# Performance work log

Hardware: AMD Instinct MI355X
Metric: run time of the kernel (lower is better)

## Reference

```python
import jax, jax.numpy as jnp
import numpy as np

N_NODES = 50000
N_EDGES = 600000
IN_DIM = 128
HID = 128


def gcn_conv(x, W, b, src, dst, num_nodes):
    """PyG-style GCNConv: add self-loops, symmetric D^-1/2 (A+I) D^-1/2 normalization."""
    xw = x @ W  # [N, H]
    loop = jnp.arange(num_nodes)
    s = jnp.concatenate([src, loop])
    d = jnp.concatenate([dst, loop])
    deg = jax.ops.segment_sum(jnp.ones_like(d, dtype=xw.dtype), d, num_segments=num_nodes)
    dinv = jax.lax.rsqrt(deg)  # deg >= 1 thanks to self-loops
    norm = dinv[s] * dinv[d]  # [E+N]
    msgs = xw[s] * norm[:, None]  # gather + scale, [E+N, H]
    out = jax.ops.segment_sum(msgs, d, num_segments=num_nodes)
    return out + b


def setup_inputs() -> dict:
    key = jax.random.key(0)
    ks = jax.random.split(key, 12)
    sc_in = 1.0 / np.sqrt(IN_DIM)
    sc_h = 1.0 / np.sqrt(HID)
    sc_2h = 1.0 / np.sqrt(2 * HID)
    return {
        "x": jax.random.normal(ks[0], (N_NODES, IN_DIM), jnp.float32),
        "hidden_state": jax.random.normal(ks[1], (N_NODES, HID), jnp.float32),
        "edge_index": jax.random.randint(ks[2], (2, N_EDGES), 0, N_NODES, dtype=jnp.int32),
        "W_in": jax.random.normal(ks[3], (IN_DIM, HID), jnp.float32) * sc_in,
        "b_in": jnp.zeros((HID,), jnp.float32),
        "W_hid": jax.random.normal(ks[4], (HID, HID), jnp.float32) * sc_h,
        "b_hid": jnp.zeros((HID,), jnp.float32),
        "W_z": jax.random.normal(ks[5], (2 * HID, HID), jnp.float32) * sc_2h,
        "b_z": jnp.zeros((HID,), jnp.float32),
        "W_r": jax.random.normal(ks[6], (2 * HID, HID), jnp.float32) * sc_2h,
        "b_r": jnp.zeros((HID,), jnp.float32),
        "W_c": jax.random.normal(ks[7], (2 * HID, HID), jnp.float32) * sc_2h,
        "b_c": jnp.zeros((HID,), jnp.float32),
    }


def reference(x, hidden_state, edge_index, W_in, b_in, W_hid, b_hid, W_z, b_z, W_r, b_r, W_c, b_c):
    src, dst = edge_index[0], edge_index[1]
    n = x.shape[0]
    # two stacked GCN layers (dropout identity in eval mode)
    h1 = jax.nn.relu(gcn_conv(x, W_in, b_in, src, dst, n))
    emb = gcn_conv(h1, W_hid, b_hid, src, dst, n)  # [N, H]
    # GRU-style gating
    combined = jnp.concatenate([emb, hidden_state], axis=1)  # [N, 2H]
    update = jax.nn.sigmoid(combined @ W_z + b_z)
    reset = jax.nn.sigmoid(combined @ W_r + b_r)
    cand_in = jnp.concatenate([emb, reset * hidden_state], axis=1)
    candidate = jnp.tanh(cand_in @ W_c + b_c)
    new_hidden = (1.0 - update) * hidden_state + update * candidate
    return new_hidden
```

## Files before the change

kernel.cpp:

```cpp
#include <hip/hip_runtime.h>
#include <cstdint>
#include <cstddef>

typedef unsigned short u16;
typedef unsigned int   u32;

typedef __bf16 bf8   __attribute__((ext_vector_type(8)));
typedef float  f32x4 __attribute__((ext_vector_type(4)));

__device__ __forceinline__ float b2f(u16 v) {
  union { u32 i; float f; } c; c.i = ((u32)v) << 16; return c.f;
}
__device__ __forceinline__ u16 f2b(float f) {
  union { u32 i; float f; } c; c.f = f;
  u32 x = c.i;
  u32 r = (x + 0x7FFFu + ((x >> 16) & 1u)) >> 16;
  return (u16)r;
}
__device__ __forceinline__ float sigf(float x) { return 1.0f / (1.0f + __expf(-x)); }
__device__ __forceinline__ float tanhfast(float x) { return 2.0f * sigf(2.0f * x) - 1.0f; }

__device__ __forceinline__ bf8 cvt8(const float* __restrict__ p) {
  f32x4 lo = *(const f32x4*)p;
  f32x4 hi = *(const f32x4*)(p + 4);
  union { u16 s[8]; bf8 v; } c;
#pragma unroll
  for (int i = 0; i < 4; ++i) { c.s[i] = f2b(lo[i]); c.s[4 + i] = f2b(hi[i]); }
  return c.v;
}
__device__ __forceinline__ bf8 asbf8(uint4 q) {
  union { uint4 q; bf8 v; } c; c.q = q; return c.v;
}

__device__ __forceinline__ void ld_lds16(const u16* g, u16* l) {
  __builtin_amdgcn_global_load_lds((const __attribute__((address_space(1))) void*)g,
                                   (__attribute__((address_space(3))) void*)l, 16, 0, 0);
}

#define CSR_STRIDE 80

__global__ __launch_bounds__(256) void k_transpose(
    const float* __restrict__ W0, const float* __restrict__ W1,
    const float* __restrict__ W2, const float* __restrict__ W3,
    const float* __restrict__ W4,
    u16* __restrict__ B0, u16* __restrict__ B1, u16* __restrict__ B2,
    u16* __restrict__ B3, u16* __restrict__ B4,
    int* __restrict__ cnt, int N) {
  if (blockIdx.x >= 64) {
    int i = (blockIdx.x - 64) * 256 + threadIdx.x;
    if (i < N) cnt[i] = 0;
    return;
  }
  int t = blockIdx.x * 256 + threadIdx.x;
  const float* in; u16* out; int f;
  if (t < 2048)       { in = W0; out = B0; f = t; }
  else if (t < 4096)  { in = W1; out = B1; f = t - 2048; }
  else if (t < 8192)  { in = W2; out = B2; f = t - 4096; }
  else if (t < 12288) { in = W3; out = B3; f = t - 8192; }
  else                { in = W4; out = B4; f = t - 12288; }
  int ln = f & 15, quad = (f >> 4) & 3, c = (f >> 6) & 7, ks = (f >> 9) & 3, hh = f >> 11;
  int n = c * 16 + ln;
  int k0 = hh * 128 + ks * 32 + quad * 8;
  union { u16 s[8]; uint4 q; } tmp;
#pragma unroll
  for (int j = 0; j < 8; ++j) tmp.s[j] = f2b(in[(size_t)(k0 + j) * 128 + n]);
  *(uint4*)(out + (size_t)f * 8) = tmp.q;
}

__global__ void k_fill(const int* __restrict__ src, const int* __restrict__ dst,
                       int* __restrict__ cnt, int* __restrict__ csr, int E) {
  int e = blockIdx.x * 256 + threadIdx.x;
  if (e < E) {
    int d = dst[e];
    int pos = atomicAdd(&cnt[d], 1);
    if (pos < CSR_STRIDE) csr[(size_t)d * CSR_STRIDE + pos] = src[e];
  }
}

__global__ __launch_bounds__(256) void k_agg(const u16* __restrict__ y,
                                             const int* __restrict__ cnt,
                                             const int* __restrict__ csr,
                                             const float* __restrict__ bias,
                                             u16* __restrict__ out, int relu, int N) {
  int wv = (blockIdx.x * 256 + threadIdx.x) >> 6;
  int lane = threadIdx.x & 63;
  if (wv >= N) return;
  int g = lane >> 4, t = lane & 15;
  const uint4* yq = (const uint4*)y;
  int deg = cnt[wv];
  int degc = (deg < 64) ? deg : 64;
  long base = (long)wv * CSR_STRIDE;
  int myidx = (lane < degc) ? csr[base + lane] : 0;

  float a[8];
#pragma unroll
  for (int j = 0; j < 8; ++j) a[j] = 0.0f;

  for (int b = 0; b < degc; b += 8) {
    int e0 = b + g, e1 = b + 4 + g;
    int s0 = __shfl(myidx, (e0 < degc) ? e0 : 0, 64);
    int s1 = __shfl(myidx, (e1 < degc) ? e1 : 0, 64);
    uint4 v0 = yq[(size_t)s0 * 16 + t];
    uint4 v1 = yq[(size_t)s1 * 16 + t];
    if (e0 < degc) {
      const u32* w = (const u32*)&v0;
#pragma unroll
      for (int i = 0; i < 4; ++i) { a[2*i] += b2f((u16)(w[i] & 0xFFFF)); a[2*i+1] += b2f((u16)(w[i] >> 16)); }
    }
    if (e1 < degc) {
      const u32* w = (const u32*)&v1;
#pragma unroll
      for (int i = 0; i < 4; ++i) { a[2*i] += b2f((u16)(w[i] & 0xFFFF)); a[2*i+1] += b2f((u16)(w[i] >> 16)); }
    }
  }
#pragma unroll
  for (int j = 0; j < 8; ++j) {
    a[j] += __shfl_xor(a[j], 16, 64);
    a[j] += __shfl_xor(a[j], 32, 64);
  }
  if (g == 0) {
    int degt = (deg < CSR_STRIDE) ? deg : CSR_STRIDE;
    for (int p = 64; p < degt; ++p) {
      int s = csr[base + p];
      uint4 v = yq[(size_t)s * 16 + t];
      const u32* w = (const u32*)&v;
#pragma unroll
      for (int i = 0; i < 4; ++i) { a[2*i] += b2f((u16)(w[i] & 0xFFFF)); a[2*i+1] += b2f((u16)(w[i] >> 16)); }
    }
    uint4 sv = yq[(size_t)wv * 16 + t];
    const u32* w = (const u32*)&sv;
#pragma unroll
    for (int i = 0; i < 4; ++i) { a[2*i] += b2f((u16)(w[i] & 0xFFFF)); a[2*i+1] += b2f((u16)(w[i] >> 16)); }
    float di = rsqrtf((float)deg + 1.0f);
    f32x4 b0 = *(const f32x4*)(bias + t * 8);
    f32x4 b1 = *(const f32x4*)(bias + t * 8 + 4);
    union { u16 s[8]; uint4 q; } o;
#pragma unroll
    for (int j = 0; j < 8; ++j) {
      float r = di * a[j] + ((j < 4) ? b0[j] : b1[j - 4]);
      if (relu) r = fmaxf(r, 0.0f);
      o.s[j] = f2b(r);
    }
    ((uint4*)out)[(size_t)wv * 16 + t] = o.q;
  }
}

template <bool AF>
__global__ __launch_bounds__(256) void k_gemm(
    const void* __restrict__ Av,
    const u16* __restrict__ Bt,
    const int* __restrict__ cnt,
    u16* __restrict__ outb, int M) {
  __shared__ __align__(16) u16 bs[16384];
  int tid = threadIdx.x;
  int lane = tid & 63, wave = tid >> 6;
  int ln = lane & 15, quad = lane >> 4;
  int rowbase = blockIdx.x * 64 + wave * 16;
  int rowA = rowbase + ln;
  long rA = (rowA < M) ? rowA : (M - 1);

  {
    const u16* g = Bt + wave * 4096 + lane * 8;
    u16* l = bs + wave * 4096;
#pragma unroll
    for (int i = 0; i < 8; ++i) ld_lds16(g + i * 512, l + i * 512);
  }

  bf8 af[4];
#pragma unroll
  for (int ks = 0; ks < 4; ++ks) {
    int kk = ks * 32 + quad * 8;
    if (AF) af[ks] = cvt8((const float*)Av + rA * 128 + kk);
    else    af[ks] = *(const bf8*)((const u16*)Av + rA * 128 + kk);
  }

  f32x4 acc[8];
#pragma unroll
  for (int c = 0; c < 8; ++c) { acc[c][0] = 0.f; acc[c][1] = 0.f; acc[c][2] = 0.f; acc[c][3] = 0.f; }

  __syncthreads();
#pragma unroll
  for (int ks = 0; ks < 4; ++ks) {
#pragma unroll
    for (int c = 0; c < 8; ++c) {
      bf8 bfr = *(const bf8*)(bs + ks * 4096 + c * 512 + lane * 8);
      acc[c] = __builtin_amdgcn_mfma_f32_16x16x32_bf16(af[ks], bfr, acc[c], 0, 0, 0);
    }
  }

  int rb = rowbase + quad * 4;
  float rs[4];
#pragma unroll
  for (int r = 0; r < 4; ++r) {
    int row = rb + r;
    rs[r] = (row < M) ? rsqrtf((float)cnt[row] + 1.0f) : 0.0f;
  }
#pragma unroll
  for (int c = 0; c < 8; ++c) {
    int col = c * 16 + ln;
#pragma unroll
    for (int r = 0; r < 4; ++r) {
      int row = rb + r;
      if (row < M) outb[(size_t)row * 128 + col] = f2b(acc[c][r] * rs[r]);
    }
  }
}

__global__ __launch_bounds__(256, 2) void k_gru(
    const u16* __restrict__ emb, const float* __restrict__ h,
    const u16* __restrict__ Btz, const u16* __restrict__ Btr, const u16* __restrict__ Btc,
    const float* __restrict__ bz, const float* __restrict__ br, const float* __restrict__ bc,
    float* __restrict__ out, int M) {
  __shared__ __align__(16) u16 at[8192];
  int tid = threadIdx.x;
  int lane = tid & 63, wave = tid >> 6;
  int ln = lane & 15, quad = lane >> 4;
  int rowbase = blockIdx.x * 64 + wave * 16;
  int rowA = rowbase + ln;
  long rA = (rowA < M) ? rowA : (M - 1);
  int rb = rowbase + quad * 4;

  const uint4* Bz = (const uint4*)Btz;
  const uint4* Br = (const uint4*)Btr;
  const uint4* Bc = (const uint4*)Btc;

  bf8 af_e[4], af_h[4];
#pragma unroll
  for (int ks = 0; ks < 4; ++ks)
    af_e[ks] = *(const bf8*)(emb + rA * 128 + ks * 32 + quad * 8);
#pragma unroll
  for (int ks = 0; ks < 4; ++ks)
    af_h[ks] = cvt8(h + rA * 128 + ks * 32 + quad * 8);

  f32x4 accz[8], accr[8];
#pragma unroll
  for (int c = 0; c < 8; ++c) {
    accz[c][0] = 0.f; accz[c][1] = 0.f; accz[c][2] = 0.f; accz[c][3] = 0.f;
    accr[c][0] = 0.f; accr[c][1] = 0.f; accr[c][2] = 0.f; accr[c][3] = 0.f;
  }

  auto loadb = [&](uint4 (&d)[8], const uint4* B, int ksg) {
#pragma unroll
    for (int c = 0; c < 8; ++c) d[c] = B[(size_t)ksg * 512 + c * 64 + lane];
  };
  auto mmzr = [&](uint4 (&cz)[8], uint4 (&cr)[8], int ksg) {
    bf8 af = (ksg < 4) ? af_e[ksg] : af_h[ksg - 4];
#pragma unroll
    for (int c = 0; c < 8; ++c) {
      accz[c] = __builtin_amdgcn_mfma_f32_16x16x32_bf16(af, asbf8(cz[c]), accz[c], 0, 0, 0);
      accr[c] = __builtin_amdgcn_mfma_f32_16x16x32_bf16(af, asbf8(cr[c]), accr[c], 0, 0, 0);
    }
  };

  uint4 z0[8], r0[8], z1[8], r1[8];
  loadb(z0, Bz, 0); loadb(r0, Br, 0);
  loadb(z1, Bz, 1); loadb(r1, Br, 1);
  mmzr(z0, r0, 0);
  loadb(z0, Bz, 2); loadb(r0, Br, 2);
  mmzr(z1, r1, 1);
  loadb(z1, Bz, 3); loadb(r1, Br, 3);
  mmzr(z0, r0, 2);
  loadb(z0, Bz, 4); loadb(r0, Br, 4);
  mmzr(z1, r1, 3);
  loadb(z1, Bz, 5); loadb(r1, Br, 5);
  mmzr(z0, r0, 4);
  loadb(z0, Bz, 6); loadb(r0, Br, 6);
  mmzr(z1, r1, 5);
  loadb(z1, Bz, 7); loadb(r1, Br, 7);
  mmzr(z0, r0, 6);
  mmzr(z1, r1, 7);

  f32x4 hc[8];
#pragma unroll
  for (int c = 0; c < 8; ++c) {
    int col = c * 16 + ln;
#pragma unroll
    for (int r = 0; r < 4; ++r) {
      int row = rb + r;
      hc[c][r] = (row < M) ? h[(size_t)row * 128 + col] : 0.0f;
    }
  }

#pragma unroll
  for (int c = 0; c < 8; ++c) {
    int col = c * 16 + ln;
    float bzc = bz[col], brc = br[col];
#pragma unroll
    for (int r = 0; r < 4; ++r) {
      float uu = sigf(accz[c][r] + bzc);
      float rr = sigf(accr[c][r] + brc);
      accz[c][r] = uu;
      int lrow = wave * 16 + quad * 4 + r;
      at[lrow * 128 + col] = f2b(rr * hc[c][r]);
      accr[c][r] = 0.0f;
    }
  }
  __syncthreads();

  bf8 af_at[4];
#pragma unroll
  for (int ks = 0; ks < 4; ++ks)
    af_at[ks] = *(const bf8*)(at + (wave * 16 + ln) * 128 + ks * 32 + quad * 8);

  auto mmc = [&](uint4 (&cc)[8], int ksg) {
    bf8 af = (ksg < 4) ? af_e[ksg] : af_at[ksg - 4];
#pragma unroll
    for (int c = 0; c < 8; ++c)
      accr[c] = __builtin_amdgcn_mfma_f32_16x16x32_bf16(af, asbf8(cc[c]), accr[c], 0, 0, 0);
  };
  uint4 c0[8], c1[8];
  loadb(c0, Bc, 0);
  loadb(c1, Bc, 1);
  mmc(c0, 0);
  loadb(c0, Bc, 2);
  mmc(c1, 1);
  loadb(c1, Bc, 3);
  mmc(c0, 2);
  loadb(c0, Bc, 4);
  mmc(c1, 3);
  loadb(c1, Bc, 5);
  mmc(c0, 4);
  loadb(c0, Bc, 6);
  mmc(c1, 5);
  loadb(c1, Bc, 7);
  mmc(c0, 6);
  mmc(c1, 7);

#pragma unroll
  for (int c = 0; c < 8; ++c) {
    int col = c * 16 + ln;
    float bcc = bc[col];
#pragma unroll
    for (int r = 0; r < 4; ++r) {
      int row = rb + r;
      if (row < M) {
        float cd = tanhfast(accr[c][r] + bcc);
        float uu = accz[c][r];
        out[(size_t)row * 128 + col] = (1.0f - uu) * hc[c][r] + uu * cd;
      }
    }
  }
}

extern "C" void kernel_launch(void* const* d_in, const int* in_sizes, int n_in,
                              void* d_out, int out_size, void* d_ws, size_t ws_size,
                              hipStream_t stream) {
  const float* x     = (const float*)d_in[0];
  const float* h     = (const float*)d_in[1];
  const int*   ei    = (const int*)d_in[2];
  const float* W_in  = (const float*)d_in[3];
  const float* b_in  = (const float*)d_in[4];
  const float* W_hid = (const float*)d_in[5];
  const float* b_hid = (const float*)d_in[6];
  const float* W_z   = (const float*)d_in[7];
  const float* b_z   = (const float*)d_in[8];
  const float* W_r   = (const float*)d_in[9];
  const float* b_r   = (const float*)d_in[10];
  const float* W_c   = (const float*)d_in[11];
  const float* b_c   = (const float*)d_in[12];

  const int N = in_sizes[0] / 128;
  const int E = in_sizes[2] / 2;
  const int* src = ei;
  const int* dst = ei + E;

  char* p = (char*)d_ws;
  auto carve = [&](size_t bytes) { char* r = p; p += (bytes + 255) & ~(size_t)255; return r; };
  u16* Bt_in   = (u16*)carve((size_t)16384 * 2);
  u16* Bt_hid  = (u16*)carve((size_t)16384 * 2);
  u16* Bt_z    = (u16*)carve((size_t)32768 * 2);
  u16* Bt_r    = (u16*)carve((size_t)32768 * 2);
  u16* Bt_c    = (u16*)carve((size_t)32768 * 2);
  int* cnt  = (int*)carve((size_t)N * 4);
  int* csr  = (int*)carve((size_t)N * CSR_STRIDE * 4);
  u16* y    = (u16*)carve((size_t)N * 128 * 2);
  u16* h1   = (u16*)carve((size_t)N * 128 * 2);
  u16* emb  = (u16*)carve((size_t)N * 128 * 2);

  int gN = (N + 255) / 256;
  int gE = (E + 255) / 256;
  int gG = (N + 63) / 64;
  int gA = (N + 3) / 4;

  k_transpose<<<64 + gN, 256, 0, stream>>>(W_in, W_hid, W_z, W_r, W_c,
                                           Bt_in, Bt_hid, Bt_z, Bt_r, Bt_c, cnt, N);
  k_fill<<<gE, 256, 0, stream>>>(src, dst, cnt, csr, E);

  k_gemm<true><<<gG, 256, 0, stream>>>(x, Bt_in, cnt, y, N);
  k_agg<<<gA, 256, 0, stream>>>(y, cnt, csr, b_in, h1, 1, N);
  k_gemm<false><<<gG, 256, 0, stream>>>(h1, Bt_hid, cnt, y, N);
  k_agg<<<gA, 256, 0, stream>>>(y, cnt, csr, b_hid, emb, 0, N);
  k_gru<<<gG, 256, 0, stream>>>(emb, h, Bt_z, Bt_r, Bt_c, b_z, b_r, b_c, (float*)d_out, N);
}
```

Measured before the change: 268.9 us.

## Give each node a 16-lane group in agg and make GRU persistent with LDS weights

The aggregation kernel now gives each node a 16-lane group instead of a full wave. It issues up to 16 neighbour row gathers at once, aiming for more memory-level parallelism and less idle lane work at the low average degree. The GRU kernel becomes a persistent 512-thread kernel that stages the z and r weight matrices in LDS once and loops over 128-row tiles, instead of reloading them from global memory per block. The hidden state is converted to bf16 inside the CSR-fill kernel to halve GRU reads. The cost is lower precision in the final blend term, possible tail imbalance across 256 blocks, and a large LDS footprint that allows one block per CU.

```diff
diff --git a/kernel.cpp b/kernel.cpp
--- a/kernel.cpp
+++ b/kernel.cpp
@@ -1,4 +1,5 @@
 #include <hip/hip_runtime.h>
+#include <hip/hip_bf16.h>
 #include <cstdint>
 #include <cstddef>
 
@@ -68,12 +69,21 @@
 }
 
 __global__ void k_fill(const int* __restrict__ src, const int* __restrict__ dst,
-                       int* __restrict__ cnt, int* __restrict__ csr, int E) {
-  int e = blockIdx.x * 256 + threadIdx.x;
-  if (e < E) {
-    int d = dst[e];
+                       int* __restrict__ cnt, int* __restrict__ csr, int E,
+                       const float* __restrict__ h, u16* __restrict__ hb, int HV8) {
+  int i = blockIdx.x * 256 + threadIdx.x;
+  if (i < E) {
+    int d = dst[i];
     int pos = atomicAdd(&cnt[d], 1);
-    if (pos < CSR_STRIDE) csr[(size_t)d * CSR_STRIDE + pos] = src[e];
+    if (pos < CSR_STRIDE) csr[(size_t)d * CSR_STRIDE + pos] = src[i];
+  }
+  if (i < HV8) {
+    const float* p = h + (size_t)i * 8;
+    f32x4 lo = *(const f32x4*)p, hi = *(const f32x4*)(p + 4);
+    union { u16 s[8]; uint4 q; } o;
+#pragma unroll
+    for (int j = 0; j < 4; ++j) { o.s[j] = f2b(lo[j]); o.s[4 + j] = f2b(hi[j]); }
+    ((uint4*)hb)[i] = o.q;
   }
 }
 
@@ -82,67 +92,63 @@
                                              const int* __restrict__ csr,
                                              const float* __restrict__ bias,
                                              u16* __restrict__ out, int relu, int N) {
-  int wv = (blockIdx.x * 256 + threadIdx.x) >> 6;
+  int gid = (blockIdx.x * 256 + threadIdx.x) >> 4;
   int lane = threadIdx.x & 63;
-  if (wv >= N) return;
-  int g = lane >> 4, t = lane & 15;
+  int t = lane & 15;
+  if (gid >= N) return;
+  int deg0 = cnt[gid];
+  int deg = (deg0 < CSR_STRIDE) ? deg0 : CSR_STRIDE;
+  long base = (long)gid * CSR_STRIDE;
   const uint4* yq = (const uint4*)y;
-  int deg = cnt[wv];
-  int degc = (deg < 64) ? deg : 64;
-  long base = (long)wv * CSR_STRIDE;
-  int myidx = (lane < degc) ? csr[base + lane] : 0;
-
-  float a[8];
-#pragma unroll
-  for (int j = 0; j < 8; ++j) a[j] = 0.0f;
-
-  for (int b = 0; b < degc; b += 8) {
-    int e0 = b + g, e1 = b + 4 + g;
-    int s0 = __shfl(myidx, (e0 < degc) ? e0 : 0, 64);
-    int s1 = __shfl(myidx, (e1 < degc) ? e1 : 0, 64);
-    uint4 v0 = yq[(size_t)s0 * 16 + t];
-    uint4 v1 = yq[(size_t)s1 * 16 + t];
-    if (e0 < degc) {
-      const u32* w = (const u32*)&v0;
-#pragma unroll
-      for (int i = 0; i < 4; ++i) { a[2*i] += b2f((u16)(w[i] & 0xFFFF)); a[2*i+1] += b2f((u16)(w[i] >> 16)); }
-    }
-    if (e1 < degc) {
-      const u32* w = (const u32*)&v1;
-#pragma unroll
-      for (int i = 0; i < 4; ++i) { a[2*i] += b2f((u16)(w[i] & 0xFFFF)); a[2*i+1] += b2f((u16)(w[i] >> 16)); }
-    }
-  }
-#pragma unroll
-  for (int j = 0; j < 8; ++j) {
-    a[j] += __shfl_xor(a[j], 16, 64);
-    a[j] += __shfl_xor(a[j], 32, 64);
-  }
-  if (g == 0) {
-    int degt = (deg < CSR_STRIDE) ? deg : CSR_STRIDE;
-    for (int p = 64; p < degt; ++p) {
-      int s = csr[base + p];
-      uint4 v = yq[(size_t)s * 16 + t];
-      const u32* w = (const u32*)&v;
-#pragma unroll
-      for (int i = 0; i < 4; ++i) { a[2*i] += b2f((u16)(w[i] & 0xFFFF)); a[2*i+1] += b2f((u16)(w[i] >> 16)); }
-    }
-    uint4 sv = yq[(size_t)wv * 16 + t];
-    const u32* w = (const u32*)&sv;
-#pragma unroll
-    for (int i = 0; i < 4; ++i) { a[2*i] += b2f((u16)(w[i] & 0xFFFF)); a[2*i+1] += b2f((u16)(w[i] >> 16)); }
-    float di = rsqrtf((float)deg + 1.0f);
-    f32x4 b0 = *(const f32x4*)(bias + t * 8);
-    f32x4 b1 = *(const f32x4*)(bias + t * 8 + 4);
-    union { u16 s[8]; uint4 q; } o;
-#pragma unroll
-    for (int j = 0; j < 8; ++j) {
-      float r = di * a[j] + ((j < 4) ? b0[j] : b1[j - 4]);
-      if (relu) r = fmaxf(r, 0.0f);
-      o.s[j] = f2b(r);
-    }
-    ((uint4*)out)[(size_t)wv * 16 + t] = o.q;
-  }
+
+  float2 a[4];
+#pragma unroll
+  for (int i = 0; i < 4; ++i) { a[i].x = 0.0f; a[i].y = 0.0f; }
+
+  uint4 sv = yq[(size_t)gid * 16 + t];
+
+  for (int j0 = 0; j0 < deg; j0 += 16) {
+    int cc = deg - j0; if (cc > 16) cc = 16;
+    int my = (t < cc) ? csr[base + j0 + t] : 0;
+    int sl[16];
+#pragma unroll
+    for (int k = 0; k < 16; ++k)
+      sl[k] = __shfl(my, (lane & 48) | ((k < cc) ? k : 0), 64);
+    uint4 v[16];
+#pragma unroll
+    for (int k = 0; k < 16; ++k) v[k] = yq[(size_t)sl[k] * 16 + t];
+#pragma unroll
+    for (int k = 0; k < 16; ++k) {
+      if (k < cc) {
+        const __hip_bfloat162* pb = (const __hip_bfloat162*)&v[k];
+#pragma unroll
+        for (int i = 0; i < 4; ++i) {
+          float2 f = __bfloat1622float2(pb[i]);
+          a[i].x += f.x; a[i].y += f.y;
+        }
+      }
+    }
+  }
+  {
+    const __hip_bfloat162* pb = (const __hip_bfloat162*)&sv;
+#pragma unroll
+    for (int i = 0; i < 4; ++i) {
+      float2 f = __bfloat1622float2(pb[i]);
+      a[i].x += f.x; a[i].y += f.y;
+    }
+  }
+  float di = rsqrtf((float)deg0 + 1.0f);
+  f32x4 b0 = *(const f32x4*)(bias + t * 8);
+  f32x4 b1 = *(const f32x4*)(bias + t * 8 + 4);
+  union { u16 s[8]; uint4 q; } o;
+#pragma unroll
+  for (int i = 0; i < 4; ++i) {
+    float r0 = di * a[i].x + ((2 * i < 4) ? b0[2 * i] : b1[2 * i - 4]);
+    float r1 = di * a[i].y + ((2 * i + 1 < 4) ? b0[2 * i + 1] : b1[2 * i - 3]);
+    if (relu) { r0 = fmaxf(r0, 0.0f); r1 = fmaxf(r1, 0.0f); }
+    o.s[2 * i] = f2b(r0); o.s[2 * i + 1] = f2b(r1);
+  }
+  ((uint4*)out)[(size_t)gid * 16 + t] = o.q;
 }
 
 template <bool AF>
@@ -206,137 +212,142 @@
   }
 }
 
-__global__ __launch_bounds__(256, 2) void k_gru(
-    const u16* __restrict__ emb, const float* __restrict__ h,
+#define AT_STRIDE 72
+__global__ __launch_bounds__(512, 1) void k_gru(
+    const u16* __restrict__ emb, const u16* __restrict__ hb,
     const u16* __restrict__ Btz, const u16* __restrict__ Btr, const u16* __restrict__ Btc,
     const float* __restrict__ bz, const float* __restrict__ br, const float* __restrict__ bc,
     float* __restrict__ out, int M) {
-  __shared__ __align__(16) u16 at[8192];
+  __shared__ __align__(16) u16 bs[65536];
+  __shared__ __align__(16) u16 at[8 * 16 * AT_STRIDE];
   int tid = threadIdx.x;
   int lane = tid & 63, wave = tid >> 6;
   int ln = lane & 15, quad = lane >> 4;
-  int rowbase = blockIdx.x * 64 + wave * 16;
-  int rowA = rowbase + ln;
-  long rA = (rowA < M) ? rowA : (M - 1);
-  int rb = rowbase + quad * 4;
-
-  const uint4* Bz = (const uint4*)Btz;
-  const uint4* Br = (const uint4*)Btr;
+  u16* atw = at + wave * 16 * AT_STRIDE;
+
+#pragma unroll
+  for (int i = 0; i < 8; ++i) {
+    int fi = i * 512 + tid;
+    ld_lds16(Btz + (size_t)fi * 8, bs + (size_t)fi * 8);
+  }
+#pragma unroll
+  for (int i = 0; i < 8; ++i) {
+    int fi = i * 512 + tid;
+    ld_lds16(Btr + (size_t)fi * 8, bs + 32768 + (size_t)fi * 8);
+  }
+  __syncthreads();
+
   const uint4* Bc = (const uint4*)Btc;
-
-  bf8 af_e[4], af_h[4];
-#pragma unroll
-  for (int ks = 0; ks < 4; ++ks)
-    af_e[ks] = *(const bf8*)(emb + rA * 128 + ks * 32 + quad * 8);
-#pragma unroll
-  for (int ks = 0; ks < 4; ++ks)
-    af_h[ks] = cvt8(h + rA * 128 + ks * 32 + quad * 8);
-
-  f32x4 accz[8], accr[8];
-#pragma unroll
-  for (int c = 0; c < 8; ++c) {
-    accz[c][0] = 0.f; accz[c][1] = 0.f; accz[c][2] = 0.f; accz[c][3] = 0.f;
-    accr[c][0] = 0.f; accr[c][1] = 0.f; accr[c][2] = 0.f; accr[c][3] = 0.f;
-  }
-
-  auto loadb = [&](uint4 (&d)[8], const uint4* B, int ksg) {
-#pragma unroll
-    for (int c = 0; c < 8; ++c) d[c] = B[(size_t)ksg * 512 + c * 64 + lane];
-  };
-  auto mmzr = [&](uint4 (&cz)[8], uint4 (&cr)[8], int ksg) {
-    bf8 af = (ksg < 4) ? af_e[ksg] : af_h[ksg - 4];
+  int numTiles = (M + 127) >> 7;
+
+  for (int tile = blockIdx.x; tile < numTiles; tile += gridDim.x) {
+    int rowbase = tile * 128 + wave * 16;
+    int rowA = rowbase + ln;
+    long rA = (rowA < M) ? rowA : (M - 1);
+    int rb = rowbase + quad * 4;
+
+    bf8 af_e[4], af_h[4];
+#pragma unroll
+    for (int ks = 0; ks < 4; ++ks) {
+      af_e[ks] = *(const bf8*)(emb + rA * 128 + ks * 32 + quad * 8);
+      af_h[ks] = *(const bf8*)(hb + rA * 128 + ks * 32 + quad * 8);
+    }
+    f32x4 hc[8];
 #pragma unroll
     for (int c = 0; c < 8; ++c) {
-      accz[c] = __builtin_amdgcn_mfma_f32_16x16x32_bf16(af, asbf8(cz[c]), accz[c], 0, 0, 0);
-      accr[c] = __builtin_amdgcn_mfma_f32_16x16x32_bf16(af, asbf8(cr[c]), accr[c], 0, 0, 0);
-    }
-  };
-
-  uint4 z0[8], r0[8], z1[8], r1[8];
-  loadb(z0, Bz, 0); loadb(r0, Br, 0);
-  loadb(z1, Bz, 1); loadb(r1, Br, 1);
-  mmzr(z0, r0, 0);
-  loadb(z0, Bz, 2); loadb(r0, Br, 2);
-  mmzr(z1, r1, 1);
-  loadb(z1, Bz, 3); loadb(r1, Br, 3);
-  mmzr(z0, r0, 2);
-  loadb(z0, Bz, 4); loadb(r0, Br, 4);
-  mmzr(z1, r1, 3);
-  loadb(z1, Bz, 5); loadb(r1, Br, 5);
-  mmzr(z0, r0, 4);
-  loadb(z0, Bz, 6); loadb(r0, Br, 6);
-  mmzr(z1, r1, 5);
-  loadb(z1, Bz, 7); loadb(r1, Br, 7);
-  mmzr(z0, r0, 6);
-  mmzr(z1, r1, 7);
-
-  f32x4 hc[8];
-#pragma unroll
-  for (int c = 0; c < 8; ++c) {
-    int col = c * 16 + ln;
-#pragma unroll
-    for (int r = 0; r < 4; ++r) {
-      int row = rb + r;
-      hc[c][r] = (row < M) ? h[(size_t)row * 128 + col] : 0.0f;
-    }
-  }
-
-#pragma unroll
-  for (int c = 0; c < 8; ++c) {
-    int col = c * 16 + ln;
-    float bzc = bz[col], brc = br[col];
-#pragma unroll
-    for (int r = 0; r < 4; ++r) {
-      float uu = sigf(accz[c][r] + bzc);
-      float rr = sigf(accr[c][r] + brc);
-      accz[c][r] = uu;
-      int lrow = wave * 16 + quad * 4 + r;
-      at[lrow * 128 + col] = f2b(rr * hc[c][r]);
-      accr[c][r] = 0.0f;
-    }
-  }
-  __syncthreads();
-
-  bf8 af_at[4];
-#pragma unroll
-  for (int ks = 0; ks < 4; ++ks)
-    af_at[ks] = *(const bf8*)(at + (wave * 16 + ln) * 128 + ks * 32 + quad * 8);
-
-  auto mmc = [&](uint4 (&cc)[8], int ksg) {
-    bf8 af = (ksg < 4) ? af_e[ksg] : af_at[ksg - 4];
-#pragma unroll
-    for (int c = 0; c < 8; ++c)
-      accr[c] = __builtin_amdgcn_mfma_f32_16x16x32_bf16(af, asbf8(cc[c]), accr[c], 0, 0, 0);
-  };
-  uint4 c0[8], c1[8];
-  loadb(c0, Bc, 0);
-  loadb(c1, Bc, 1);
-  mmc(c0, 0);
-  loadb(c0, Bc, 2);
-  mmc(c1, 1);
-  loadb(c1, Bc, 3);
-  mmc(c0, 2);
-  loadb(c0, Bc, 4);
-  mmc(c1, 3);
-  loadb(c1, Bc, 5);
-  mmc(c0, 4);
-  loadb(c0, Bc, 6);
-  mmc(c1, 5);
-  loadb(c1, Bc, 7);
-  mmc(c0, 6);
-  mmc(c1, 7);
-
-#pragma unroll
-  for (int c = 0; c < 8; ++c) {
-    int col = c * 16 + ln;
-    float bcc = bc[col];
-#pragma unroll
-    for (int r = 0; r < 4; ++r) {
-      int row = rb + r;
-      if (row < M) {
-        float cd = tanhfast(accr[c][r] + bcc);
-        float uu = accz[c][r];
-        out[(size_t)row * 128 + col] = (1.0f - uu) * hc[c][r] + uu * cd;
+      int col = c * 16 + ln;
+#pragma unroll
+      for (int r = 0; r < 4; ++r) {
+        int row = rb + r;
+        hc[c][r] = (row < M) ? b2f(hb[(size_t)row * 128 + col]) : 0.0f;
+      }
+    }
+
+    f32x4 accz[8], accr[8];
+#pragma unroll
+    for (int c = 0; c < 8; ++c) {
+      accz[c][0] = 0.f; accz[c][1] = 0.f; accz[c][2] = 0.f; accz[c][3] = 0.f;
+      accr[c][0] = 0.f; accr[c][1] = 0.f; accr[c][2] = 0.f; accr[c][3] = 0.f;
+    }
+
+#pragma unroll
+    for (int ksg = 0; ksg < 8; ++ksg) {
+      bf8 af = (ksg < 4) ? af_e[ksg] : af_h[ksg - 4];
+#pragma unroll
+      for (int c = 0; c < 8; ++c) {
+        bf8 vz = *(const bf8*)(bs + ((size_t)ksg * 512 + c * 64 + lane) * 8);
+        accz[c] = __builtin_amdgcn_mfma_f32_16x16x32_bf16(af, vz, accz[c], 0, 0, 0);
+        bf8 vr = *(const bf8*)(bs + 32768 + ((size_t)ksg * 512 + c * 64 + lane) * 8);
+        accr[c] = __builtin_amdgcn_mfma_f32_16x16x32_bf16(af, vr, accr[c], 0, 0, 0);
+      }
+    }
+
+    bf8 af_at[4];
+#pragma unroll
+    for (int c = 0; c < 4; ++c) {
+      int col = c * 16 + ln;
+      float bzc = bz[col], brc = br[col];
+#pragma unroll
+      for (int r = 0; r < 4; ++r) {
+        float uu = sigf(accz[c][r] + bzc);
+        float rr = sigf(accr[c][r] + brc);
+        accz[c][r] = uu;
+        atw[(quad * 4 + r) * AT_STRIDE + col] = f2b(rr * hc[c][r]);
+        accr[c][r] = 0.0f;
+      }
+    }
+#pragma unroll
+    for (int ks = 0; ks < 2; ++ks)
+      af_at[ks] = *(const bf8*)(atw + ln * AT_STRIDE + ks * 32 + quad * 8);
+#pragma unroll
+    for (int c = 4; c < 8; ++c) {
+      int col = c * 16 + ln;
+      float bzc = bz[col], brc = br[col];
+#pragma unroll
+      for (int r = 0; r < 4; ++r) {
+        float uu = sigf(accz[c][r] + bzc);
+        float rr = sigf(accr[c][r] + brc);
+        accz[c][r] = uu;
+        atw[(quad * 4 + r) * AT_STRIDE + (col - 64)] = f2b(rr * hc[c][r]);
+        accr[c][r] = 0.0f;
+      }
+    }
+#pragma unroll
+    for (int ks = 2; ks < 4; ++ks)
+      af_at[ks] = *(const bf8*)(atw + ln * AT_STRIDE + (ks - 2) * 32 + quad * 8);
+
+    uint4 cb[2][8];
+    auto loadc = [&](int buf, int ksg) {
+#pragma unroll
+      for (int c = 0; c < 8; ++c) cb[buf][c] = Bc[(size_t)ksg * 512 + c * 64 + lane];
+    };
+    auto mfc = [&](int buf, int ksg) {
+      bf8 af = (ksg < 4) ? af_e[ksg] : af_at[ksg - 4];
+#pragma unroll
+      for (int c = 0; c < 8; ++c)
+        accr[c] = __builtin_amdgcn_mfma_f32_16x16x32_bf16(af, asbf8(cb[buf][c]), accr[c], 0, 0, 0);
+    };
+    loadc(0, 0); loadc(1, 1);
+    mfc(0, 0); loadc(0, 2);
+    mfc(1, 1); loadc(1, 3);
+    mfc(0, 2); loadc(0, 4);
+    mfc(1, 3); loadc(1, 5);
+    mfc(0, 4); loadc(0, 6);
+    mfc(1, 5); loadc(1, 7);
+    mfc(0, 6); mfc(1, 7);
+
+#pragma unroll
+    for (int c = 0; c < 8; ++c) {
+      int col = c * 16 + ln;
+      float bcc = bc[col];
+#pragma unroll
+      for (int r = 0; r < 4; ++r) {
+        int row = rb + r;
+        if (row < M) {
+          float cd = tanhfast(accr[c][r] + bcc);
+          float uu = accz[c][r];
+          out[(size_t)row * 128 + col] = (1.0f - uu) * hc[c][r] + uu * cd;
+        }
       }
     }
   }
@@ -376,19 +387,22 @@
   u16* y    = (u16*)carve((size_t)N * 128 * 2);
   u16* h1   = (u16*)carve((size_t)N * 128 * 2);
   u16* emb  = (u16*)carve((size_t)N * 128 * 2);
+  u16* hb   = (u16*)carve((size_t)N * 128 * 2);
 
   int gN = (N + 255) / 256;
-  int gE = (E + 255) / 256;
+  int HV8 = N * 16;
+  int gF = (HV8 + 255) / 256;
+  if (gF < (E + 255) / 256) gF = (E + 255) / 256;
   int gG = (N + 63) / 64;
-  int gA = (N + 3) / 4;
+  int gA = (N + 15) / 16;
 
   k_transpose<<<64 + gN, 256, 0, stream>>>(W_in, W_hid, W_z, W_r, W_c,
                                            Bt_in, Bt_hid, Bt_z, Bt_r, Bt_c, cnt, N);
-  k_fill<<<gE, 256, 0, stream>>>(src, dst, cnt, csr, E);
+  k_fill<<<gF, 256, 0, stream>>>(src, dst, cnt, csr, E, h, hb, HV8);
 
   k_gemm<true><<<gG, 256, 0, stream>>>(x, Bt_in, cnt, y, N);
   k_agg<<<gA, 256, 0, stream>>>(y, cnt, csr, b_in, h1, 1, N);
   k_gemm<false><<<gG, 256, 0, stream>>>(h1, Bt_hid, cnt, y, N);
   k_agg<<<gA, 256, 0, stream>>>(y, cnt, csr, b_hid, emb, 0, N);
-  k_gru<<<gG, 256, 0, stream>>>(emb, h, Bt_z, Bt_r, Bt_c, b_z, b_r, b_c, (float*)d_out, N);
-}
+  k_gru<<<256, 512, 0, stream>>>(emb, hb, Bt_z, Bt_r, Bt_c, b_z, b_r, b_c, (float*)d_out, N);
+}
```

After: 533.3 us. 1.98x slower.
